# Optimization experiments

Measured on AMD Instinct MI355X. Metric: run time of the kernel, lower is better.

Reference implementation:

```python
import jax, jax.numpy as jnp
import numpy as np

B, T, E, V, L = 8, 128, 256, 8192, 5  # batch, block_size, embedding_size (== num heads, head_size=1), vocab, num blocks


def setup_inputs() -> dict:
    key = jax.random.key(0)
    ks = jax.random.split(key, 12)
    s = 0.02
    return {
        "idxs": jax.random.randint(ks[0], (B, T), 0, V),
        "targets": jax.random.randint(ks[1], (B, T), 0, V),
        "emb": jax.random.normal(ks[2], (V, E)) * s,
        "pos_emb": jax.random.normal(ks[3], (T, E)) * s,
        "Wq": jax.random.normal(ks[4], (L, E, E)) * s,  # per-layer: E heads, each Linear(E,1); columns are heads
        "Wk": jax.random.normal(ks[5], (L, E, E)) * s,
        "Wv": jax.random.normal(ks[6], (L, E, E)) * s,
        "Wfc": jax.random.normal(ks[7], (L, E, E)) * s,
        "bfc": jnp.zeros((L, E)),
        "Wlm": jax.random.normal(ks[8], (E, V)) * s,
        "blm": jnp.zeros((V,)),
    }


def _block(x, Wq, Wk, Wv, Wfc, bfc):
    # E heads of head_size=1: projecting with [E,E] gives [B,T,H] with H==E,
    # column h being head h's scalar q/k/v. Faithful to per-head Linear(E,1).
    q = x @ Wq
    k = x @ Wk
    v = x @ Wv
    scores = jnp.einsum('bih,bjh->bhij', q, k)  # no 1/sqrt(d) scaling (faithful)
    i = jnp.arange(x.shape[1])
    causal = i[:, None] >= i[None, :]  # masked_fill where tril==0, i.e. j>i -> -inf
    scores = jnp.where(causal[None, None], scores, -jnp.inf)
    attn = jax.nn.softmax(scores, axis=-2)  # NOTE: source softmaxes over dim=-2 (query axis) -- faithful quirk
    out = jnp.einsum('bhij,bjh->bih', attn, v)  # concat of heads == H axis order
    x = x + out
    return x + jax.nn.relu(x @ Wfc + bfc)


def reference(idxs, targets, emb, pos_emb, Wq, Wk, Wv, Wfc, bfc, Wlm, blm):
    x = emb[idxs] + pos_emb[: idxs.shape[1]]  # [B,T,E]
    for l in range(L):
        x = _block(x, Wq[l], Wk[l], Wv[l], Wfc[l], bfc[l])
    logits = (x @ Wlm + blm).reshape(-1, V)  # [B*T, V], as source views before CE
    logp = jax.nn.log_softmax(logits, axis=-1)
    loss = -jnp.take_along_axis(logp, targets.reshape(-1, 1), axis=-1).mean()
    return logits, loss
```

## Files before the change

### kernel.cpp

```cpp
#include <hip/hip_runtime.h>

#define BB 8
#define TT 128
#define EE 256
#define VV 8192
#define LL 5
#define NROWS (BB*TT)

typedef __attribute__((ext_vector_type(8))) short bf16x8;
typedef __attribute__((ext_vector_type(4))) float f32x4;

__device__ inline ushort f2bf(float f) {
    union { float f; unsigned u; } c; c.f = f;
    unsigned u = c.u;
    return (ushort)((u + 0x7FFF + ((u >> 16) & 1)) >> 16);
}
__device__ inline float bf2f(ushort u) {
    union { unsigned u; float f; } c; c.u = ((unsigned)u) << 16;
    return c.f;
}

__device__ __forceinline__ void gload_lds16(const void* g, void* l) {
    __builtin_amdgcn_global_load_lds((const __attribute__((address_space(1))) unsigned int*)g,
                                     (__attribute__((address_space(3))) unsigned int*)l,
                                     16, 0, 0);
}


__global__ __launch_bounds__(512, 2) void layer0_kernel(
        const int* __restrict__ idxs, const float* __restrict__ emb, const float* __restrict__ pos,
        const float* __restrict__ Wq, const float* __restrict__ Wk,
        const float* __restrict__ Wv, const float* __restrict__ Wfc,
        const float* __restrict__ Wlm,
        float* __restrict__ y_out, ushort* __restrict__ WTs, ushort* __restrict__ WlmT,
        float* __restrict__ loss_cell) {
    __shared__ __align__(16) ushort Xs[128*128];
    __shared__ __align__(16) ushort Bs[32*128];
    __shared__ __align__(16) float QS[8*132], KS[8*132], VS[8*132], MS[8*132];
    int tid = threadIdx.x, lane = tid & 63, w = tid >> 6;
    int blk = blockIdx.x;

    if (blk >= 256) {
        int id = blk - 256;
        if (id == 0) {
            if (tid == 0) *loss_cell = 0.f;
            return;
        }
        ushort (*ts)[72] = (ushort(*)[72])Xs;
        if (id < 513) {
            int idw = id - 1;
            int v0 = (idw & 127) * 64, k0 = (idw >> 7) * 64;
            for (int kk = w; kk < 64; kk += 8)
                ts[lane][kk] = f2bf(Wlm[(size_t)(k0 + kk)*VV + v0 + lane]);
            __syncthreads();
            for (int vv = w; vv < 64; vv += 8) {
                int r = v0 + vv, k = k0 + lane;
                WlmT[(size_t)r*256 + (k & 128) + ((k & 127) ^ ((r & 7) << 3))] = ts[vv][lane];
            }
            return;
        }
        {
            int idm = id - 513;
            int mat = idm >> 4, tile = idm & 15;
            int l = mat >> 2, type = mat & 3;
            const float* src = (type == 0 ? Wq : type == 1 ? Wk : type == 2 ? Wv : Wfc) + l*EE*EE;
            ushort* dst = WTs + mat*EE*EE;
            int i0 = (tile >> 2) * 64, o0 = (tile & 3) * 64;
            for (int ii = w; ii < 64; ii += 8)
                ts[lane][ii] = f2bf(src[(i0 + ii)*EE + o0 + lane]);
            __syncthreads();
            for (int oo = w; oo < 64; oo += 8) {
                int r = o0 + oo, k = i0 + lane;
                dst[(size_t)r*256 + (k & 128) + ((k & 127) ^ ((r & 7) << 3))] = ts[oo][lane];
            }
            return;
        }
    }

    int b  = blk >> 5;
    int h0 = (blk & 31) * 8;

    f32x4 acc[2] = {};
    int rband = w*16 + (lane & 15);
    int kq = (lane >> 4) * 8;

    #pragma unroll
    for (int half = 0; half < 2; ++half) {
        if (half) __syncthreads();
        {
            int rsub = lane >> 5, cb = (lane & 31) * 4;
            for (int rr2 = w*2; rr2 < 128; rr2 += 16) {
                int rr = rr2 + rsub;
                int id = idxs[b*TT + rr];
                float4 v = *(const float4*)&emb[(size_t)id*EE + half*128 + cb];
                float4 p = *(const float4*)&pos[rr*EE + half*128 + cb];
                ushort4 hh;
                hh.x = f2bf(v.x + p.x); hh.y = f2bf(v.y + p.y);
                hh.z = f2bf(v.z + p.z); hh.w = f2bf(v.w + p.w);
                *(ushort4*)&Xs[rr*128 + (cb ^ ((rr & 7) << 3))] = hh;
            }
        }
        {
            int c = tid >> 4;
            int kb8 = (tid & 15) * 8;
            ushort tmp[8];
            if (c < 24) {
                int mat = c >> 3;
                int col = h0 + (c & 7);
                const float* Wm = mat == 0 ? Wq : (mat == 1 ? Wk : Wv);
                #pragma unroll
                for (int i = 0; i < 8; ++i)
                    tmp[i] = f2bf(Wm[(size_t)(half*128 + kb8 + i)*EE + col]);
            } else {
                #pragma unroll
                for (int i = 0; i < 8; ++i) tmp[i] = 0;
            }
            ushort* dst = &Bs[c*128 + (kb8 ^ ((c & 7) << 3))];
            *(ushort4*)dst       = *(ushort4*)&tmp[0];
            *(ushort4*)(dst + 4) = *(ushort4*)&tmp[4];
        }
        __syncthreads();
        for (int ks = 0; ks < 4; ++ks) {
            int kk = ks*32 + kq;
            bf16x8 a = *(const bf16x8*)&Xs[rband*128 + (kk ^ ((rband & 7) << 3))];
            #pragma unroll
            for (int ct = 0; ct < 2; ++ct) {
                int c = ct*16 + (lane & 15);
                bf16x8 bb = *(const bf16x8*)&Bs[c*128 + (kk ^ ((c & 7) << 3))];
                acc[ct] = __builtin_amdgcn_mfma_f32_16x16x32_bf16(a, bb, acc[ct], 0, 0, 0);
            }
        }
    }
    {
        int r_ = w*16 + ((lane >> 4) << 2);
        #pragma unroll
        for (int ct = 0; ct < 2; ++ct) {
            int col24 = ct*16 + (lane & 15);
            #pragma unroll
            for (int j = 0; j < 4; ++j) {
                float val = acc[ct][j];
                int row = r_ + j;
                if (col24 < 8)       QS[col24*132 + row] = val;
                else if (col24 < 16) KS[(col24-8)*132 + row] = val;
                else if (col24 < 24) VS[(col24-16)*132 + row] = val;
            }
        }
    }
    __syncthreads();

    int g = w, lg = lane;
    {
        int j0 = lg*2;
        float k0 = KS[g*132 + j0], k1 = KS[g*132 + j0 + 1];
        float q0j = QS[g*132 + j0], q1j = QS[g*132 + j0 + 1];
        float pmax = fmaxf(q0j, q1j), pmin = fminf(q0j, q1j);
        #pragma unroll
        for (int d = 1; d < 64; d <<= 1) {
            float om = __shfl_down(pmax, d);
            float on = __shfl_down(pmin, d);
            if (lg + d < 64) { pmax = fmaxf(pmax, om); pmin = fminf(pmin, on); }
        }
        float nx = __shfl_down(pmax, 1), nn = __shfl_down(pmin, 1);
        float sp1 = (lg == 63) ? q1j : fmaxf(q1j, nx);
        float sn1 = (lg == 63) ? q1j : fminf(q1j, nn);
        MS[g*132 + j0]     = (k0 >= 0.f) ? k0*pmax : k0*pmin;
        MS[g*132 + j0 + 1] = (k1 >= 0.f) ? k1*sp1  : k1*sn1;
    }
    __syncthreads();

    {
        float outp[32];
        #pragma unroll
        for (int r = 0; r < 32; ++r) outp[r] = 0.f;
        int c = lg & 15, rg = lg >> 4;
        int rbase = rg * 32;
        for (int jt = 0; jt < 8; ++jt) {
            int j = jt*16 + c;
            float kj = KS[g*132 + j];
            float mj = MS[g*132 + j];
            float vj = VS[g*132 + j];
            float P[32];
            float z = 0.f;
            #pragma unroll
            for (int r = 0; r < 32; ++r) {
                int i = rbase + r;
                float e = __expf(QS[g*132 + i] * kj - mj);
                e = (i >= j) ? e : 0.f;
                P[r] = e;
                z += e;
            }
            z += __shfl_xor(z, 16);
            z += __shfl_xor(z, 32);
            float rv = vj / z;
            #pragma unroll
            for (int r = 0; r < 32; ++r) outp[r] += P[r] * rv;
        }
        #pragma unroll
        for (int r = 0; r < 32; ++r) {
            float v = outp[r];
            v += __shfl_xor(v, 1);
            v += __shfl_xor(v, 2);
            v += __shfl_xor(v, 4);
            v += __shfl_xor(v, 8);
            outp[r] = v;
        }
        __syncthreads();
        if (c == 0) {
            #pragma unroll
            for (int r = 0; r < 32; ++r)
                VS[g*132 + rbase + r] = outp[r];
        }
    }
    __syncthreads();

    {
        int row = tid >> 2, cp = (tid & 3) * 2;
        int id = idxs[b*TT + row];
        float2 ev = *(const float2*)&emb[(size_t)id*EE + h0 + cp];
        float2 pv = *(const float2*)&pos[row*EE + h0 + cp];
        float2 ov;
        ov.x = ev.x + pv.x + VS[cp*132 + row];
        ov.y = ev.y + pv.y + VS[(cp+1)*132 + row];
        *(float2*)&y_out[(size_t)(b*TT + row)*EE + h0 + cp] = ov;
    }
}

__global__ __launch_bounds__(512, 2) void layer_kernel(
        const float* __restrict__ y_in, float* __restrict__ y_out,
        const ushort* __restrict__ WTfc, const float* __restrict__ bfc_prev,
        const ushort* __restrict__ WTqkv) {
    __shared__ __align__(16) ushort Zbuf[128*256];
    __shared__ __align__(16) ushort Ybuf[128*256];
    __shared__ __align__(16) char U[25600];
    ushort* BsF = (ushort*)U;
    ushort* Bsq = (ushort*)U;
    float* QS = (float*)(U + 8192);
    float* KS = QS + 8*132;
    float* VS = KS + 8*132;
    float* MS = VS + 8*132;
    int tid = threadIdx.x, lane = tid & 63, w = tid >> 6;
    int b  = blockIdx.x >> 5;
    int h0 = (blockIdx.x & 31) * 8;
    int rband = w*16 + (lane & 15);
    int kq = (lane >> 4) * 8;

    for (int rr = w; rr < 128; rr += 8) {
        float4 v = *(const float4*)&y_in[(size_t)(b*TT + rr)*EE + lane*4];
        ushort4 hh;
        hh.x = f2bf(v.x); hh.y = f2bf(v.y); hh.z = f2bf(v.z); hh.w = f2bf(v.w);
        int k0 = lane*4;
        *(ushort4*)&Ybuf[rr*256 + (k0 & 128) + ((k0 & 127) ^ ((rr & 7) << 3))] = hh;
    }
    __syncthreads();

    f32x4 accz[4][4] = {};
    #pragma unroll
    for (int half = 0; half < 2; ++half) {
        #pragma unroll
        for (int cg = 0; cg < 4; ++cg) {
            __syncthreads();
            {
                int rg0 = w*8;
                const ushort* s0 = WTfc + (size_t)(cg*64 + rg0 + (lane >> 4))*256
                                 + half*128 + (lane & 15)*8;
                gload_lds16(s0, &BsF[(size_t)rg0*128]);
                const ushort* s1 = WTfc + (size_t)(cg*64 + rg0 + 4 + (lane >> 4))*256
                                 + half*128 + (lane & 15)*8;
                gload_lds16(s1, &BsF[(size_t)(rg0 + 4)*128]);
            }
            __syncthreads();
            for (int ks = 0; ks < 4; ++ks) {
                int kk = ks*32 + kq;
                bf16x8 a = *(const bf16x8*)&Ybuf[rband*256 + half*128 + (kk ^ ((rband & 7) << 3))];
                #pragma unroll
                for (int n = 0; n < 4; ++n) {
                    int c = n*16 + (lane & 15);
                    bf16x8 bb = *(const bf16x8*)&BsF[c*128 + (kk ^ ((c & 7) << 3))];
                    accz[cg][n] = __builtin_amdgcn_mfma_f32_16x16x32_bf16(a, bb, accz[cg][n], 0, 0, 0);
                }
            }
        }
    }
    {
        int grow0 = w*16 + ((lane >> 4) << 2);
        #pragma unroll
        for (int cg = 0; cg < 4; ++cg) {
            #pragma unroll
            for (int n = 0; n < 4; ++n) {
                int col = cg*64 + n*16 + (lane & 15);
                float bias = bfc_prev[col];
                int coff = (col & 128), csub = col & 127;
                #pragma unroll
                for (int j = 0; j < 4; ++j) {
                    int row = grow0 + j;
                    int sw = coff + (csub ^ ((row & 7) << 3));
                    float y = bf2f(Ybuf[row*256 + sw]);
                    float z = y + fmaxf(accz[cg][n][j] + bias, 0.f);
                    Zbuf[row*256 + sw] = f2bf(z);
                }
            }
        }
    }
    __syncthreads();

    f32x4 acc[2] = {};
    #pragma unroll
    for (int half = 0; half < 2; ++half) {
        if (half) __syncthreads();
        {
            int rowg = w*4 + (lane >> 4);
            int rowv = rowg < 24 ? rowg : 23;
            int mat = rowv >> 3, col = h0 + (rowv & 7);
            const ushort* src = WTqkv + (size_t)mat*EE*EE + (size_t)col*256
                              + half*128 + (lane & 15)*8;
            gload_lds16(src, &Bsq[(size_t)w*4*128]);
        }
        __syncthreads();
        for (int ks = 0; ks < 4; ++ks) {
            int kk = ks*32 + kq;
            bf16x8 a = *(const bf16x8*)&Zbuf[rband*256 + half*128 + (kk ^ ((rband & 7) << 3))];
            #pragma unroll
            for (int ct = 0; ct < 2; ++ct) {
                int c = ct*16 + (lane & 15);
                bf16x8 bb = *(const bf16x8*)&Bsq[c*128 + (kk ^ ((c & 7) << 3))];
                acc[ct] = __builtin_amdgcn_mfma_f32_16x16x32_bf16(a, bb, acc[ct], 0, 0, 0);
            }
        }
    }
    {
        int r_ = w*16 + ((lane >> 4) << 2);
        #pragma unroll
        for (int ct = 0; ct < 2; ++ct) {
            int col24 = ct*16 + (lane & 15);
            #pragma unroll
            for (int j = 0; j < 4; ++j) {
                float val = acc[ct][j];
                int row = r_ + j;
                if (col24 < 8)       QS[col24*132 + row] = val;
                else if (col24 < 16) KS[(col24-8)*132 + row] = val;
                else if (col24 < 24) VS[(col24-16)*132 + row] = val;
            }
        }
    }
    __syncthreads();

    int g = w, lg = lane;
    {
        int j0 = lg*2;
        float k0 = KS[g*132 + j0], k1 = KS[g*132 + j0 + 1];
        float q0j = QS[g*132 + j0], q1j = QS[g*132 + j0 + 1];
        float pmax = fmaxf(q0j, q1j), pmin = fminf(q0j, q1j);
        #pragma unroll
        for (int d = 1; d < 64; d <<= 1) {
            float om = __shfl_down(pmax, d);
            float on = __shfl_down(pmin, d);
            if (lg + d < 64) { pmax = fmaxf(pmax, om); pmin = fminf(pmin, on); }
        }
        float nx = __shfl_down(pmax, 1), nn = __shfl_down(pmin, 1);
        float sp1 = (lg == 63) ? q1j : fmaxf(q1j, nx);
        float sn1 = (lg == 63) ? q1j : fminf(q1j, nn);
        MS[g*132 + j0]     = (k0 >= 0.f) ? k0*pmax : k0*pmin;
        MS[g*132 + j0 + 1] = (k1 >= 0.f) ? k1*sp1  : k1*sn1;
    }
    __syncthreads();
    {
        float outp[32];
        #pragma unroll
        for (int r = 0; r < 32; ++r) outp[r] = 0.f;
        int c = lg & 15, rg = lg >> 4;
        int rbase = rg * 32;
        for (int jt = 0; jt < 8; ++jt) {
            int j = jt*16 + c;
            float kj = KS[g*132 + j];
            float mj = MS[g*132 + j];
            float vj = VS[g*132 + j];
            float P[32];
            float z = 0.f;
            #pragma unroll
            for (int r = 0; r < 32; ++r) {
                int i = rbase + r;
                float e = __expf(QS[g*132 + i] * kj - mj);
                e = (i >= j) ? e : 0.f;
                P[r] = e;
                z += e;
            }
            z += __shfl_xor(z, 16);
            z += __shfl_xor(z, 32);
            float rv = vj / z;
            #pragma unroll
            for (int r = 0; r < 32; ++r) outp[r] += P[r] * rv;
        }
        #pragma unroll
        for (int r = 0; r < 32; ++r) {
            float v = outp[r];
            v += __shfl_xor(v, 1);
            v += __shfl_xor(v, 2);
            v += __shfl_xor(v, 4);
            v += __shfl_xor(v, 8);
            outp[r] = v;
        }
        __syncthreads();
        if (c == 0) {
            #pragma unroll
            for (int r = 0; r < 32; ++r)
                VS[g*132 + rbase + r] = outp[r];
        }
    }
    __syncthreads();

    {
        int row = tid >> 2, cp = (tid & 3) * 2;
        int c0i = h0 + cp, c1i = h0 + cp + 1;
        float z0 = bf2f(Zbuf[row*256 + (c0i & 128) + ((c0i & 127) ^ ((row & 7) << 3))]);
        float z1 = bf2f(Zbuf[row*256 + (c1i & 128) + ((c1i & 127) ^ ((row & 7) << 3))]);
        float2 ov;
        ov.x = z0 + VS[cp*132 + row];
        ov.y = z1 + VS[(cp+1)*132 + row];
        *(float2*)&y_out[(size_t)(b*TT + row)*EE + h0 + cp] = ov;
    }
}

__global__ __launch_bounds__(256, 4) void fc_mfma(
        const float* __restrict__ xin, const ushort* __restrict__ WT,
        const float* __restrict__ bfc, float* __restrict__ xout) {
    __shared__ __align__(16) ushort As[64*128];
    __shared__ __align__(16) ushort Bs[64*128];
    int tid = threadIdx.x, lane = tid & 63, w = tid >> 6;
    int c0 = blockIdx.x * 64;
    int r0 = blockIdx.y * 64;

    f32x4 acc[4] = {};
    int rband = w*16 + (lane & 15);
    int kq = (lane >> 4) * 8;

    #pragma unroll
    for (int half = 0; half < 2; ++half) {
        if (half) __syncthreads();
        {
            int rsub = lane >> 5, cb = (lane & 31) * 4;
            for (int rr2 = w*2; rr2 < 64; rr2 += 8) {
                int rr = rr2 + rsub;
                float4 v = *(const float4*)&xin[(size_t)(r0 + rr)*EE + half*128 + cb];
                ushort4 hh; hh.x = f2bf(v.x); hh.y = f2bf(v.y); hh.z = f2bf(v.z); hh.w = f2bf(v.w);
                *(ushort4*)&As[rr*128 + (cb ^ ((rr & 7) << 3))] = hh;
            }
        }
        for (int rg = w*4; rg < 64; rg += 16) {
            int row = c0 + rg + (lane >> 4);
            const ushort* src = WT + (size_t)row*256 + half*128 + (lane & 15)*8;
            gload_lds16(src, &Bs[(size_t)rg*128]);
        }
        __syncthreads();
        for (int ks = 0; ks < 4; ++ks) {
            int kk = ks*32 + kq;
            bf16x8 a = *(const bf16x8*)&As[rband*128 + (kk ^ ((rband & 7) << 3))];
            #pragma unroll
            for (int n = 0; n < 4; ++n) {
                int c = n*16 + (lane & 15);
                bf16x8 b = *(const bf16x8*)&Bs[c*128 + (kk ^ ((c & 7) << 3))];
                acc[n] = __builtin_amdgcn_mfma_f32_16x16x32_bf16(a, b, acc[n], 0, 0, 0);
            }
        }
    }
    int grow0 = r0 + w*16 + ((lane >> 4) << 2);
    #pragma unroll
    for (int n = 0; n < 4; ++n) {
        int col = c0 + n*16 + (lane & 15);
        float bias = bfc[col];
        #pragma unroll
        for (int j = 0; j < 4; ++j) {
            size_t idx = (size_t)(grow0 + j)*EE + col;
            xout[idx] = xin[idx] + fmaxf(acc[n][j] + bias, 0.f);
        }
    }
}

__global__ __launch_bounds__(512, 4) void lm_mfma_kernel(
        const float* __restrict__ x, const ushort* __restrict__ WlmT,
        const float* __restrict__ blm, float* __restrict__ out,
        float* __restrict__ pm, float* __restrict__ pz) {
    __shared__ __align__(16) char LDSb[128*132*4];
    ushort* As = (ushort*)LDSb;
    ushort* Bs = (ushort*)LDSb + 128*128;
    float*  fst = (float*)LDSb;
    int tid = threadIdx.x;
    int lane = tid & 63, w = tid >> 6;
    int c0 = blockIdx.x * 128;
    int r0 = blockIdx.y * 128;

    int wr = (w >> 2) * 64, wc = (w & 3) * 32;
    f32x4 acc[4][2] = {};
    int kq = (lane >> 4) * 8;

    #pragma unroll
    for (int half = 0; half < 2; ++half) {
        if (half) __syncthreads();
        {
            int rsub = lane >> 5, cb = (lane & 31) * 4;
            for (int rr2 = w*2; rr2 < 128; rr2 += 16) {
                int rr = rr2 + rsub;
                float4 v = *(const float4*)&x[(size_t)(r0 + rr)*EE + half*128 + cb];
                ushort4 hh; hh.x = f2bf(v.x); hh.y = f2bf(v.y); hh.z = f2bf(v.z); hh.w = f2bf(v.w);
                *(ushort4*)&As[rr*128 + (cb ^ ((rr & 7) << 3))] = hh;
            }
        }
        for (int rg = w*4; rg < 128; rg += 32) {
            int row = c0 + rg + (lane >> 4);
            const ushort* src = WlmT + (size_t)row*256 + half*128 + (lane & 15)*8;
            gload_lds16(src, &Bs[(size_t)rg*128]);
        }
        __syncthreads();
        for (int ks = 0; ks < 4; ++ks) {
            int kk = ks*32 + kq;
            bf16x8 a[4], bfr[2];
            #pragma unroll
            for (int m = 0; m < 4; ++m) {
                int rband = wr + m*16 + (lane & 15);
                a[m] = *(const bf16x8*)&As[rband*128 + (kk ^ ((rband & 7) << 3))];
            }
            #pragma unroll
            for (int n = 0; n < 2; ++n) {
                int c = wc + n*16 + (lane & 15);
                bfr[n] = *(const bf16x8*)&Bs[c*128 + (kk ^ ((c & 7) << 3))];
            }
            #pragma unroll
            for (int m = 0; m < 4; ++m)
                #pragma unroll
                for (int n = 0; n < 2; ++n)
                    acc[m][n] = __builtin_amdgcn_mfma_f32_16x16x32_bf16(a[m], bfr[n], acc[m][n], 0, 0, 0);
        }
    }
    __syncthreads();

    float bias[2];
    #pragma unroll
    for (int n = 0; n < 2; ++n) bias[n] = blm[c0 + wc + n*16 + (lane & 15)];
    #pragma unroll
    for (int m = 0; m < 4; ++m) {
        int rw = wr + m*16 + (lane >> 4)*4;
        #pragma unroll
        for (int j = 0; j < 4; ++j) {
            int row = rw + j;
            float vals[2];
            float vmax = -INFINITY;
            #pragma unroll
            for (int n = 0; n < 2; ++n) {
                vals[n] = acc[m][n][j] + bias[n];
                fst[row*132 + wc + n*16 + (lane & 15)] = vals[n];
                vmax = fmaxf(vmax, vals[n]);
            }
            #pragma unroll
            for (int msk = 1; msk <= 8; msk <<= 1) vmax = fmaxf(vmax, __shfl_xor(vmax, msk));
            float z = 0.f;
            #pragma unroll
            for (int n = 0; n < 2; ++n) z += __expf(vals[n] - vmax);
            #pragma unroll
            for (int msk = 1; msk <= 8; msk <<= 1) z += __shfl_xor(z, msk);
            if ((lane & 15) == 0) {
                pm[(size_t)(r0 + row)*256 + blockIdx.x*4 + (w & 3)] = vmax;
                pz[(size_t)(r0 + row)*256 + blockIdx.x*4 + (w & 3)] = z;
            }
        }
    }
    __syncthreads();
    #pragma unroll
    for (int it = 0; it < 8; ++it) {
        int k = tid + it*512;
        int row = k >> 5, c4 = (k & 31)*4;
        float4 v = *(float4*)&fst[row*132 + c4];
        *(float4*)&out[(size_t)(r0 + row)*VV + c0 + c4] = v;
    }
}

__global__ void loss_kernel(const float* __restrict__ pm, const float* __restrict__ pz,
                            const float* __restrict__ logits, const int* __restrict__ targets,
                            float* __restrict__ out_last) {
    int r = blockIdx.x;
    int t = threadIdx.x;
    __shared__ float sm[256], sz[256];
    float m = pm[(size_t)r*256 + t];
    float z = pz[(size_t)r*256 + t];
    sm[t] = m; __syncthreads();
    for (int s = 128; s > 0; s >>= 1) {
        if (t < s) sm[t] = fmaxf(sm[t], sm[t + s]);
        __syncthreads();
    }
    float M = sm[0];
    sz[t] = z * __expf(m - M); __syncthreads();
    for (int s = 128; s > 0; s >>= 1) {
        if (t < s) sz[t] += sz[t + s];
        __syncthreads();
    }
    if (t == 0) {
        float lse = M + logf(sz[0]);
        atomicAdd(out_last, (lse - logits[(size_t)r*VV + targets[r]]) * (1.0f / NROWS));
    }
}

extern "C" void kernel_launch(void* const* d_in, const int* in_sizes, int n_in,
                              void* d_out, int out_size, void* d_ws, size_t ws_size,
                              hipStream_t stream) {
    const int*   idxs    = (const int*)d_in[0];
    const int*   targets = (const int*)d_in[1];
    const float* emb     = (const float*)d_in[2];
    const float* pos     = (const float*)d_in[3];
    const float* Wq      = (const float*)d_in[4];
    const float* Wk      = (const float*)d_in[5];
    const float* Wv      = (const float*)d_in[6];
    const float* Wfc     = (const float*)d_in[7];
    const float* bfc     = (const float*)d_in[8];
    const float* Wlm     = (const float*)d_in[9];
    const float* blm     = (const float*)d_in[10];
    float* out = (float*)d_out;
    float* loss_cell = out + (size_t)NROWS * VV;

    float* ws = (float*)d_ws;
    float*  ya   = ws;
    float*  yb   = ya + NROWS*EE;
    float*  pm   = yb + NROWS*EE;
    float*  pz   = pm + NROWS*256;
    ushort* WTs  = (ushort*)(pz + NROWS*256);
    ushort* WlmT = WTs + 20*EE*EE;

    layer0_kernel<<<1089, 512, 0, stream>>>(idxs, emb, pos, Wq, Wk, Wv, Wfc, Wlm,
                                            ya, WTs, WlmT, loss_cell);

    for (int l = 1; l < LL; ++l) {
        const float* yi = (l & 1) ? ya : yb;
        float*       yo = (l & 1) ? yb : ya;
        layer_kernel<<<256, 512, 0, stream>>>(
            yi, yo,
            WTs + (size_t)((l-1)*4 + 3)*EE*EE, bfc + (size_t)(l-1)*EE,
            WTs + (size_t)l*4*EE*EE);
    }
    fc_mfma<<<dim3(4, 16), 256, 0, stream>>>(ya, WTs + (size_t)(4*4 + 3)*EE*EE,
                                             bfc + 4*EE, yb);

    lm_mfma_kernel<<<dim3(VV/128, NROWS/128), 512, 0, stream>>>(yb, WlmT, blm, out, pm, pz);
    loss_kernel<<<NROWS, 256, 0, stream>>>(pm, pz, out, targets, loss_cell);
}
```

Baseline: 196.8 us.

## Shrink layer_kernel LDS to raise occupancy and load QKV weights in one pass

Drops the separate Zbuf by writing the FC residual output in place into Ybuf, shrinks the union scratch buffer, and removes the MS array by passing the per-key max through wave shuffles. Shared memory falls from about 156KB to about 80KB per block, so launch bounds ask for 4 blocks per CU instead of 2. The QKV weight slice is now loaded into LDS in one pass instead of two halves, which removes a sync round. The in-place overwrite of Ybuf depends on each thread reading and writing only the same elements, and the higher occupancy target may force register spilling.

```diff
diff --git a/kernel.cpp b/kernel.cpp
--- a/kernel.cpp
+++ b/kernel.cpp
@@ -225,19 +225,17 @@
     }
 }
 
-__global__ __launch_bounds__(512, 2) void layer_kernel(
+__global__ __launch_bounds__(512, 4) void layer_kernel(
         const float* __restrict__ y_in, float* __restrict__ y_out,
         const ushort* __restrict__ WTfc, const float* __restrict__ bfc_prev,
         const ushort* __restrict__ WTqkv) {
-    __shared__ __align__(16) ushort Zbuf[128*256];
     __shared__ __align__(16) ushort Ybuf[128*256];
-    __shared__ __align__(16) char U[25600];
+    __shared__ __align__(16) char U[16384];
     ushort* BsF = (ushort*)U;
     ushort* Bsq = (ushort*)U;
-    float* QS = (float*)(U + 8192);
+    float* QS = (float*)U;
     float* KS = QS + 8*132;
     float* VS = KS + 8*132;
-    float* MS = VS + 8*132;
     int tid = threadIdx.x, lane = tid & 63, w = tid >> 6;
     int b  = blockIdx.x >> 5;
     int h0 = (blockIdx.x & 31) * 8;
@@ -251,7 +249,6 @@
         int k0 = lane*4;
         *(ushort4*)&Ybuf[rr*256 + (k0 & 128) + ((k0 & 127) ^ ((rr & 7) << 3))] = hh;
     }
-    __syncthreads();
 
     f32x4 accz[4][4] = {};
     #pragma unroll
@@ -296,37 +293,39 @@
                     int sw = coff + (csub ^ ((row & 7) << 3));
                     float y = bf2f(Ybuf[row*256 + sw]);
                     float z = y + fmaxf(accz[cg][n][j] + bias, 0.f);
-                    Zbuf[row*256 + sw] = f2bf(z);
+                    Ybuf[row*256 + sw] = f2bf(z);
                 }
             }
         }
     }
-    __syncthreads();
-
+
+    __syncthreads();
+    {
+        int r0i = w*4 + (lane >> 5);
+        int rv0 = r0i < 24 ? r0i : 23;
+        const ushort* s0 = WTqkv + (size_t)(rv0 >> 3)*EE*EE + (size_t)(h0 + (rv0 & 7))*256
+                         + (lane & 31)*8;
+        gload_lds16(s0, &Bsq[(size_t)(w*4)*256]);
+        int r1i = r0i + 2;
+        int rv1 = r1i < 24 ? r1i : 23;
+        const ushort* s1 = WTqkv + (size_t)(rv1 >> 3)*EE*EE + (size_t)(h0 + (rv1 & 7))*256
+                         + (lane & 31)*8;
+        gload_lds16(s1, &Bsq[(size_t)(w*4 + 2)*256]);
+    }
+    __syncthreads();
     f32x4 acc[2] = {};
-    #pragma unroll
-    for (int half = 0; half < 2; ++half) {
-        if (half) __syncthreads();
-        {
-            int rowg = w*4 + (lane >> 4);
-            int rowv = rowg < 24 ? rowg : 23;
-            int mat = rowv >> 3, col = h0 + (rowv & 7);
-            const ushort* src = WTqkv + (size_t)mat*EE*EE + (size_t)col*256
-                              + half*128 + (lane & 15)*8;
-            gload_lds16(src, &Bsq[(size_t)w*4*128]);
-        }
-        __syncthreads();
-        for (int ks = 0; ks < 4; ++ks) {
-            int kk = ks*32 + kq;
-            bf16x8 a = *(const bf16x8*)&Zbuf[rband*256 + half*128 + (kk ^ ((rband & 7) << 3))];
-            #pragma unroll
-            for (int ct = 0; ct < 2; ++ct) {
-                int c = ct*16 + (lane & 15);
-                bf16x8 bb = *(const bf16x8*)&Bsq[c*128 + (kk ^ ((c & 7) << 3))];
-                acc[ct] = __builtin_amdgcn_mfma_f32_16x16x32_bf16(a, bb, acc[ct], 0, 0, 0);
-            }
-        }
-    }
+    for (int ks = 0; ks < 8; ++ks) {
+        int kk = ks*32 + kq;
+        bf16x8 a = *(const bf16x8*)&Ybuf[rband*256 + (kk & 128) + ((kk & 127) ^ ((rband & 7) << 3))];
+        #pragma unroll
+        for (int ct = 0; ct < 2; ++ct) {
+            int c = ct*16 + (lane & 15);
+            bf16x8 bb = *(const bf16x8*)&Bsq[c*256 + (kk & 128) + ((kk & 127) ^ ((c & 7) << 3))];
+            acc[ct] = __builtin_amdgcn_mfma_f32_16x16x32_bf16(a, bb, acc[ct], 0, 0, 0);
+        }
+    }
+    __syncthreads();
+
     {
         int r_ = w*16 + ((lane >> 4) << 2);
         #pragma unroll
@@ -345,6 +344,7 @@
     __syncthreads();
 
     int g = w, lg = lane;
+    float m0, m1;
     {
         int j0 = lg*2;
         float k0 = KS[g*132 + j0], k1 = KS[g*132 + j0 + 1];
@@ -359,10 +359,9 @@
         float nx = __shfl_down(pmax, 1), nn = __shfl_down(pmin, 1);
         float sp1 = (lg == 63) ? q1j : fmaxf(q1j, nx);
         float sn1 = (lg == 63) ? q1j : fminf(q1j, nn);
-        MS[g*132 + j0]     = (k0 >= 0.f) ? k0*pmax : k0*pmin;
-        MS[g*132 + j0 + 1] = (k1 >= 0.f) ? k1*sp1  : k1*sn1;
-    }
-    __syncthreads();
+        m0 = (k0 >= 0.f) ? k0*pmax : k0*pmin;
+        m1 = (k1 >= 0.f) ? k1*sp1  : k1*sn1;
+    }
     {
         float outp[32];
         #pragma unroll
@@ -371,8 +370,11 @@
         int rbase = rg * 32;
         for (int jt = 0; jt < 8; ++jt) {
             int j = jt*16 + c;
+            int srcl = jt*8 + (c >> 1);
+            float me = __shfl(m0, srcl);
+            float mo = __shfl(m1, srcl);
+            float mj = (c & 1) ? mo : me;
             float kj = KS[g*132 + j];
-            float mj = MS[g*132 + j];
             float vj = VS[g*132 + j];
             float P[32];
             float z = 0.f;
@@ -411,8 +413,8 @@
     {
         int row = tid >> 2, cp = (tid & 3) * 2;
         int c0i = h0 + cp, c1i = h0 + cp + 1;
-        float z0 = bf2f(Zbuf[row*256 + (c0i & 128) + ((c0i & 127) ^ ((row & 7) << 3))]);
-        float z1 = bf2f(Zbuf[row*256 + (c1i & 128) + ((c1i & 127) ^ ((row & 7) << 3))]);
+        float z0 = bf2f(Ybuf[row*256 + (c0i & 128) + ((c0i & 127) ^ ((row & 7) << 3))]);
+        float z1 = bf2f(Ybuf[row*256 + (c1i & 128) + ((c1i & 127) ^ ((row & 7) << 3))]);
         float2 ov;
         ov.x = z0 + VS[cp*132 + row];
         ov.y = z1 + VS[(cp+1)*132 + row];
```

Result: slower. 206.4 us (+4.9%).
